# Kernel optimization log

Measured on AMD Instinct MI355X. Metric: run time of the kernel, lower is better.

The kernel has to match this reference:

```python
import jax, jax.numpy as jnp
import numpy as np

NUM_EXPERTS = 64
TOPK = 2  # moe_router_topk


def setup_inputs() -> dict:
    key = jax.random.key(0)
    k1, k2 = jax.random.split(key)
    # [seq, batch, hidden] as in Megatron
    hidden_states = jax.random.normal(k1, (2048, 4, 4096), dtype=jnp.float32)
    # gating weight: Linear(hidden -> num_experts), no bias
    router_weight = jax.random.normal(k2, (NUM_EXPERTS, 4096), dtype=jnp.float32) * 0.02
    return {"hidden_states": hidden_states, "router_weight": router_weight}


def reference(hidden_states, router_weight):
    S, B, H = hidden_states.shape
    x = hidden_states.reshape(-1, H)  # [T, H], T = S*B tokens
    # Router gating is always done in fp32 in Megatron.
    logits = jnp.einsum('th,eh->te', x.astype(jnp.float32),
                        router_weight.astype(jnp.float32))  # [T, E]
    # top-k routing (moe_router_pre_softmax=False): top-k over logits,
    # then softmax over the selected k logits.
    top_vals, top_idx = jax.lax.top_k(logits, TOPK)        # [T, k]
    top_probs = jax.nn.softmax(top_vals, axis=-1)          # [T, k]
    T, E = logits.shape
    rows = jnp.arange(T)[:, None]                          # [T, 1]
    # dense probs: selected probs scattered back, zeros elsewhere
    probs = jnp.zeros((T, E), dtype=logits.dtype).at[rows, top_idx].set(top_probs)
    # boolean routing map [T, E]
    routing_map = jnp.zeros((T, E), dtype=bool).at[rows, top_idx].set(True)
    return probs, routing_map
```

## Files before the change

### kernel.cpp

```cpp
#include <hip/hip_runtime.h>
#include <math.h>


#define HDIM 4096
#define NEXP 64
#define NTOK 8192
#define HG 8
#define HSLAB (HDIM / HG)
#define KK 16
#define NCH (HSLAB / KK)
#define TPBK 64
#define XS 68

__global__ __launch_bounds__(64, 1) void logits_kernel(
        const float* __restrict__ X, const float* __restrict__ W,
        float* __restrict__ part) {
    const int tg   = blockIdx.x >> 3;
    const int hg   = blockIdx.x & 7;
    const int lane = threadIdx.x;
    const int tr   = lane >> 3;
    const int ec   = lane & 7;

    __shared__ __align__(16) float smem[2 * KK * XS];
    float* xs = smem;
    float* ws = smem + KK * XS;

    const int token0 = tg * TPBK;
    const int hbase  = hg * HSLAB;

    const int r4 = lane >> 2;
    const int sl = lane & 3;

    float acc[8][8];
    #pragma unroll
    for (int i = 0; i < 8; ++i)
        #pragma unroll
        for (int j = 0; j < 8; ++j) acc[i][j] = 0.f;

    const float* Xb = X + (size_t)token0 * HDIM + hbase;

    float4 pfx[4], pfw[4];
    #pragma unroll
    for (int p = 0; p < 4; ++p) {
        int row = p * 16 + r4;
        pfx[p] = *reinterpret_cast<const float4*>(Xb + (size_t)row * HDIM + sl * 4);
    }
    #pragma unroll
    for (int q = 0; q < 4; ++q) {
        int idx = q * 64 + lane;
        int e = idx >> 2, s2 = idx & 3;
        pfw[q] = *reinterpret_cast<const float4*>(W + (size_t)e * HDIM + hbase + s2 * 4);
    }
    #pragma unroll
    for (int p = 0; p < 4; ++p) {
        int row = p * 16 + r4;
        xs[(sl * 4 + 0) * XS + row] = pfx[p].x;
        xs[(sl * 4 + 1) * XS + row] = pfx[p].y;
        xs[(sl * 4 + 2) * XS + row] = pfx[p].z;
        xs[(sl * 4 + 3) * XS + row] = pfx[p].w;
    }
    #pragma unroll
    for (int q = 0; q < 4; ++q) {
        int idx = q * 64 + lane;
        int e = idx >> 2, s2 = idx & 3;
        ws[(s2 * 4 + 0) * XS + e] = pfw[q].x;
        ws[(s2 * 4 + 1) * XS + e] = pfw[q].y;
        ws[(s2 * 4 + 2) * XS + e] = pfw[q].z;
        ws[(s2 * 4 + 3) * XS + e] = pfw[q].w;
    }
    __syncthreads();

    for (int c = 0; c < NCH; ++c) {
        if (c + 1 < NCH) {
            const int off = (c + 1) * KK;
            #pragma unroll
            for (int p = 0; p < 4; ++p) {
                int row = p * 16 + r4;
                pfx[p] = *reinterpret_cast<const float4*>(
                    Xb + (size_t)row * HDIM + off + sl * 4);
            }
            #pragma unroll
            for (int q = 0; q < 4; ++q) {
                int idx = q * 64 + lane;
                int e = idx >> 2, s2 = idx & 3;
                pfw[q] = *reinterpret_cast<const float4*>(
                    W + (size_t)e * HDIM + hbase + off + s2 * 4);
            }
        }
        #pragma unroll
        for (int k = 0; k < KK; ++k) {
            const float4* xr = reinterpret_cast<const float4*>(xs + k * XS + tr * 8);
            const float4* wr = reinterpret_cast<const float4*>(ws + k * XS + ec * 8);
            float4 xa = xr[0], xb = xr[1];
            float4 wa = wr[0], wb = wr[1];
            float xv[8] = {xa.x, xa.y, xa.z, xa.w, xb.x, xb.y, xb.z, xb.w};
            float wv[8] = {wa.x, wa.y, wa.z, wa.w, wb.x, wb.y, wb.z, wb.w};
            #pragma unroll
            for (int i = 0; i < 8; ++i)
                #pragma unroll
                for (int j = 0; j < 8; ++j)
                    acc[i][j] = fmaf(xv[i], wv[j], acc[i][j]);
        }
        __syncthreads();
        if (c + 1 < NCH) {
            #pragma unroll
            for (int p = 0; p < 4; ++p) {
                int row = p * 16 + r4;
                xs[(sl * 4 + 0) * XS + row] = pfx[p].x;
                xs[(sl * 4 + 1) * XS + row] = pfx[p].y;
                xs[(sl * 4 + 2) * XS + row] = pfx[p].z;
                xs[(sl * 4 + 3) * XS + row] = pfx[p].w;
            }
            #pragma unroll
            for (int q = 0; q < 4; ++q) {
                int idx = q * 64 + lane;
                int e = idx >> 2, s2 = idx & 3;
                ws[(s2 * 4 + 0) * XS + e] = pfw[q].x;
                ws[(s2 * 4 + 1) * XS + e] = pfw[q].y;
                ws[(s2 * 4 + 2) * XS + e] = pfw[q].z;
                ws[(s2 * 4 + 3) * XS + e] = pfw[q].w;
            }
        }
        __syncthreads();
    }

    float* dst = part + ((size_t)hg * NTOK + token0) * NEXP;
    #pragma unroll
    for (int i = 0; i < 8; ++i) {
        int t = tr * 8 + i;
        *reinterpret_cast<float4*>(dst + (size_t)t * NEXP + ec * 8) =
            make_float4(acc[i][0], acc[i][1], acc[i][2], acc[i][3]);
        *reinterpret_cast<float4*>(dst + (size_t)t * NEXP + ec * 8 + 4) =
            make_float4(acc[i][4], acc[i][5], acc[i][6], acc[i][7]);
    }
}

__global__ __launch_bounds__(256) void topk_kernel(
        const float* __restrict__ part, float* __restrict__ probs,
        float* __restrict__ rmap) {
    const int wave = threadIdx.x >> 6;
    const int lane = threadIdx.x & 63;
    const int token = blockIdx.x * 4 + wave;

    const float* p = part + (size_t)token * NEXP + lane;
    float v = 0.f;
    #pragma unroll
    for (int hg = 0; hg < HG; ++hg) v += p[(size_t)hg * NTOK * NEXP];

    float m1 = v; int i1 = lane;
    #pragma unroll
    for (int s = 32; s > 0; s >>= 1) {
        float om = __shfl_xor(m1, s, 64);
        int   oi = __shfl_xor(i1, s, 64);
        if (om > m1 || (om == m1 && oi < i1)) { m1 = om; i1 = oi; }
    }
    float vx = (lane == i1) ? -INFINITY : v;
    float m2 = vx; int i2 = lane;
    #pragma unroll
    for (int s = 32; s > 0; s >>= 1) {
        float om = __shfl_xor(m2, s, 64);
        int   oi = __shfl_xor(i2, s, 64);
        if (om > m2 || (om == m2 && oi < i2)) { m2 = om; i2 = oi; }
    }

    float e2 = expf(m2 - m1);
    float p1 = 1.f / (1.f + e2);
    float p2 = 1.f - p1;

    float prob = (lane == i1) ? p1 : ((lane == i2) ? p2 : 0.f);
    float flag = (lane == i1 || lane == i2) ? 1.f : 0.f;
    probs[(size_t)token * NEXP + lane] = prob;
    rmap [(size_t)token * NEXP + lane] = flag;
}

extern "C" void kernel_launch(void* const* d_in, const int* in_sizes, int n_in,
                              void* d_out, int out_size, void* d_ws, size_t ws_size,
                              hipStream_t stream) {
    const float* X = (const float*)d_in[0];
    const float* W = (const float*)d_in[1];
    float* out  = (float*)d_out;
    float* part = (float*)d_ws;

    logits_kernel<<<128 * HG, 64, 0, stream>>>(X, W, part);
    topk_kernel<<<NTOK / 4, 256, 0, stream>>>(part, out, out + (size_t)NTOK * NEXP);
}
```

Measured before the change: 225.1 us.

## Split each block's hidden slab across two waves with LDS reduction

```diff
diff --git a/kernel.cpp b/kernel.cpp
--- a/kernel.cpp
+++ b/kernel.cpp
@@ -7,26 +7,28 @@
 #define NTOK 8192
 #define HG 8
 #define HSLAB (HDIM / HG)
+#define HSLABW (HSLAB / 2)
 #define KK 16
-#define NCH (HSLAB / KK)
+#define NCH (HSLABW / KK)
 #define TPBK 64
 #define XS 68
 
-__global__ __launch_bounds__(64, 1) void logits_kernel(
+__global__ __launch_bounds__(128) void logits_kernel(
         const float* __restrict__ X, const float* __restrict__ W,
         float* __restrict__ part) {
     const int tg   = blockIdx.x >> 3;
     const int hg   = blockIdx.x & 7;
-    const int lane = threadIdx.x;
+    const int wav  = threadIdx.x >> 6;
+    const int lane = threadIdx.x & 63;
     const int tr   = lane >> 3;
     const int ec   = lane & 7;
 
-    __shared__ __align__(16) float smem[2 * KK * XS];
-    float* xs = smem;
-    float* ws = smem + KK * XS;
+    __shared__ __align__(16) float smem[2 * 2 * KK * XS];
+    float* xs = smem + wav * (2 * KK * XS);
+    float* ws = xs + KK * XS;
 
     const int token0 = tg * TPBK;
-    const int hbase  = hg * HSLAB;
+    const int hbase  = hg * HSLAB + wav * HSLABW;
 
     const int r4 = lane >> 2;
     const int sl = lane & 3;
@@ -124,14 +126,31 @@
         __syncthreads();
     }
 
-    float* dst = part + ((size_t)hg * NTOK + token0) * NEXP;
-    #pragma unroll
-    for (int i = 0; i < 8; ++i) {
-        int t = tr * 8 + i;
-        *reinterpret_cast<float4*>(dst + (size_t)t * NEXP + ec * 8) =
-            make_float4(acc[i][0], acc[i][1], acc[i][2], acc[i][3]);
-        *reinterpret_cast<float4*>(dst + (size_t)t * NEXP + ec * 8 + 4) =
-            make_float4(acc[i][4], acc[i][5], acc[i][6], acc[i][7]);
+    __syncthreads();
+    if (wav == 1) {
+        #pragma unroll
+        for (int i = 0; i < 8; ++i) {
+            *reinterpret_cast<float4*>(smem + (i * 2 + 0) * 256 + lane * 4) =
+                make_float4(acc[i][0], acc[i][1], acc[i][2], acc[i][3]);
+            *reinterpret_cast<float4*>(smem + (i * 2 + 1) * 256 + lane * 4) =
+                make_float4(acc[i][4], acc[i][5], acc[i][6], acc[i][7]);
+        }
+    }
+    __syncthreads();
+    if (wav == 0) {
+        float* dst = part + ((size_t)hg * NTOK + token0) * NEXP;
+        #pragma unroll
+        for (int i = 0; i < 8; ++i) {
+            float4 r0 = *reinterpret_cast<const float4*>(smem + (i * 2 + 0) * 256 + lane * 4);
+            float4 r1 = *reinterpret_cast<const float4*>(smem + (i * 2 + 1) * 256 + lane * 4);
+            int t = tr * 8 + i;
+            *reinterpret_cast<float4*>(dst + (size_t)t * NEXP + ec * 8) =
+                make_float4(acc[i][0] + r0.x, acc[i][1] + r0.y,
+                            acc[i][2] + r0.z, acc[i][3] + r0.w);
+            *reinterpret_cast<float4*>(dst + (size_t)t * NEXP + ec * 8 + 4) =
+                make_float4(acc[i][4] + r1.x, acc[i][5] + r1.y,
+                            acc[i][6] + r1.z, acc[i][7] + r1.w);
+        }
     }
 }
 
@@ -181,6 +200,6 @@
     float* out  = (float*)d_out;
     float* part = (float*)d_ws;
 
-    logits_kernel<<<128 * HG, 64, 0, stream>>>(X, W, part);
+    logits_kernel<<<128 * HG, 128, 0, stream>>>(X, W, part);
     topk_kernel<<<NTOK / 4, 256, 0, stream>>>(part, out, out + (size_t)NTOK * NEXP);
 }
```

Measured after the change: 231.1 us. 1.03x slower.

## Pre-transpose router weights and stream them from global into registers

Applied to the files above, without the earlier changes.

```diff
diff --git a/kernel.cpp b/kernel.cpp
--- a/kernel.cpp
+++ b/kernel.cpp
@@ -12,8 +12,25 @@
 #define TPBK 64
 #define XS 68
 
-__global__ __launch_bounds__(64, 1) void logits_kernel(
-        const float* __restrict__ X, const float* __restrict__ W,
+__global__ __launch_bounds__(64) void wtrans_kernel(
+        const float* __restrict__ W, float* __restrict__ Wt) {
+    __shared__ float t[64][65];
+    const int kb = blockIdx.x * 64;
+    const int lane = threadIdx.x;
+    #pragma unroll
+    for (int q = 0; q < 16; ++q) {
+        float4 v = *reinterpret_cast<const float4*>(W + (size_t)lane * HDIM + kb + q * 4);
+        t[lane][q * 4 + 0] = v.x; t[lane][q * 4 + 1] = v.y;
+        t[lane][q * 4 + 2] = v.z; t[lane][q * 4 + 3] = v.w;
+    }
+    __syncthreads();
+    #pragma unroll 4
+    for (int k = 0; k < 64; ++k)
+        Wt[(size_t)(kb + k) * NEXP + lane] = t[lane][k];
+}
+
+__global__ __launch_bounds__(64) void logits_kernel(
+        const float* __restrict__ X, const float* __restrict__ Wt,
         float* __restrict__ part) {
     const int tg   = blockIdx.x >> 3;
     const int hg   = blockIdx.x & 7;
@@ -21,9 +38,7 @@
     const int tr   = lane >> 3;
     const int ec   = lane & 7;
 
-    __shared__ __align__(16) float smem[2 * KK * XS];
-    float* xs = smem;
-    float* ws = smem + KK * XS;
+    __shared__ __align__(16) float xs[KK * XS];
 
     const int token0 = tg * TPBK;
     const int hbase  = hg * HSLAB;
@@ -38,18 +53,13 @@
         for (int j = 0; j < 8; ++j) acc[i][j] = 0.f;
 
     const float* Xb = X + (size_t)token0 * HDIM + hbase;
-
-    float4 pfx[4], pfw[4];
+    const float* Wb = Wt + (size_t)hbase * NEXP + ec * 8;
+
+    float4 pfx[4];
     #pragma unroll
     for (int p = 0; p < 4; ++p) {
         int row = p * 16 + r4;
         pfx[p] = *reinterpret_cast<const float4*>(Xb + (size_t)row * HDIM + sl * 4);
-    }
-    #pragma unroll
-    for (int q = 0; q < 4; ++q) {
-        int idx = q * 64 + lane;
-        int e = idx >> 2, s2 = idx & 3;
-        pfw[q] = *reinterpret_cast<const float4*>(W + (size_t)e * HDIM + hbase + s2 * 4);
     }
     #pragma unroll
     for (int p = 0; p < 4; ++p) {
@@ -59,16 +69,20 @@
         xs[(sl * 4 + 2) * XS + row] = pfx[p].z;
         xs[(sl * 4 + 3) * XS + row] = pfx[p].w;
     }
-    #pragma unroll
-    for (int q = 0; q < 4; ++q) {
-        int idx = q * 64 + lane;
-        int e = idx >> 2, s2 = idx & 3;
-        ws[(s2 * 4 + 0) * XS + e] = pfw[q].x;
-        ws[(s2 * 4 + 1) * XS + e] = pfw[q].y;
-        ws[(s2 * 4 + 2) * XS + e] = pfw[q].z;
-        ws[(s2 * 4 + 3) * XS + e] = pfw[q].w;
-    }
     __syncthreads();
+
+    float4 fw0[4], fw1[4];
+    #pragma unroll
+    for (int k = 0; k < 4; ++k) {
+        const float4* wr = reinterpret_cast<const float4*>(Wb + (size_t)k * NEXP);
+        fw0[k] = wr[0]; fw1[k] = wr[1];
+    }
+    float4 fx0[2], fx1[2];
+    #pragma unroll
+    for (int k = 0; k < 2; ++k) {
+        const float4* xr = reinterpret_cast<const float4*>(xs + k * XS + tr * 8);
+        fx0[k] = xr[0]; fx1[k] = xr[1];
+    }
 
     for (int c = 0; c < NCH; ++c) {
         if (c + 1 < NCH) {
@@ -79,27 +93,28 @@
                 pfx[p] = *reinterpret_cast<const float4*>(
                     Xb + (size_t)row * HDIM + off + sl * 4);
             }
-            #pragma unroll
-            for (int q = 0; q < 4; ++q) {
-                int idx = q * 64 + lane;
-                int e = idx >> 2, s2 = idx & 3;
-                pfw[q] = *reinterpret_cast<const float4*>(
-                    W + (size_t)e * HDIM + hbase + off + s2 * 4);
-            }
         }
         #pragma unroll
         for (int k = 0; k < KK; ++k) {
-            const float4* xr = reinterpret_cast<const float4*>(xs + k * XS + tr * 8);
-            const float4* wr = reinterpret_cast<const float4*>(ws + k * XS + ec * 8);
-            float4 xa = xr[0], xb = xr[1];
-            float4 wa = wr[0], wb = wr[1];
-            float xv[8] = {xa.x, xa.y, xa.z, xa.w, xb.x, xb.y, xb.z, xb.w};
-            float wv[8] = {wa.x, wa.y, wa.z, wa.w, wb.x, wb.y, wb.z, wb.w};
+            float xv[8] = {fx0[k % 2].x, fx0[k % 2].y, fx0[k % 2].z, fx0[k % 2].w,
+                           fx1[k % 2].x, fx1[k % 2].y, fx1[k % 2].z, fx1[k % 2].w};
+            float wv[8] = {fw0[k % 4].x, fw0[k % 4].y, fw0[k % 4].z, fw0[k % 4].w,
+                           fw1[k % 4].x, fw1[k % 4].y, fw1[k % 4].z, fw1[k % 4].w};
             #pragma unroll
             for (int i = 0; i < 8; ++i)
                 #pragma unroll
                 for (int j = 0; j < 8; ++j)
                     acc[i][j] = fmaf(xv[i], wv[j], acc[i][j]);
+            {
+                int kn = c * KK + k + 4;
+                if (kn >= HSLAB) kn = HSLAB - 1;
+                const float4* wr = reinterpret_cast<const float4*>(Wb + (size_t)kn * NEXP);
+                fw0[k % 4] = wr[0]; fw1[k % 4] = wr[1];
+            }
+            if (k + 2 < KK) {
+                const float4* xr = reinterpret_cast<const float4*>(xs + (k + 2) * XS + tr * 8);
+                fx0[k % 2] = xr[0]; fx1[k % 2] = xr[1];
+            }
         }
         __syncthreads();
         if (c + 1 < NCH) {
@@ -111,17 +126,15 @@
                 xs[(sl * 4 + 2) * XS + row] = pfx[p].z;
                 xs[(sl * 4 + 3) * XS + row] = pfx[p].w;
             }
-            #pragma unroll
-            for (int q = 0; q < 4; ++q) {
-                int idx = q * 64 + lane;
-                int e = idx >> 2, s2 = idx & 3;
-                ws[(s2 * 4 + 0) * XS + e] = pfw[q].x;
-                ws[(s2 * 4 + 1) * XS + e] = pfw[q].y;
-                ws[(s2 * 4 + 2) * XS + e] = pfw[q].z;
-                ws[(s2 * 4 + 3) * XS + e] = pfw[q].w;
-            }
         }
         __syncthreads();
+        if (c + 1 < NCH) {
+            #pragma unroll
+            for (int k = 0; k < 2; ++k) {
+                const float4* xr = reinterpret_cast<const float4*>(xs + k * XS + tr * 8);
+                fx0[k] = xr[0]; fx1[k] = xr[1];
+            }
+        }
     }
 
     float* dst = part + ((size_t)hg * NTOK + token0) * NEXP;
@@ -180,7 +193,9 @@
     const float* W = (const float*)d_in[1];
     float* out  = (float*)d_out;
     float* part = (float*)d_ws;
-
-    logits_kernel<<<128 * HG, 64, 0, stream>>>(X, W, part);
+    float* Wt   = out;
+
+    wtrans_kernel<<<HDIM / 64, 64, 0, stream>>>(W, Wt);
+    logits_kernel<<<128 * HG, 64, 0, stream>>>(X, Wt, part);
     topk_kernel<<<NTOK / 4, 256, 0, stream>>>(part, out, out + (size_t)NTOK * NEXP);
 }
```

After: 239.7 us. +6.5%, slower.
